# Optimization experiments

Measured on AMD Instinct MI355X. Metric: run time of the kernel, lower is better.

The kernel has to match this reference:

```python
import jax, jax.numpy as jnp
import numpy as np

L, D, H, DFF, WIN, NS = 6, 1024, 16, 4096, 5, 8
HD = D // H
EPS = 1e-5


def setup_inputs() -> dict:
    key = jax.random.key(0)
    ks = iter(jax.random.split(key, 32))
    std = 0.02
    inp = {
        "x": jax.random.normal(next(ks), (2, 1024, D), dtype=jnp.float32),
        "Wqkv": jax.random.normal(next(ks), (L, D, 3 * D), dtype=jnp.float32) * std,
        "bqkv": jnp.zeros((L, 3 * D), jnp.float32),
        "Wo": jax.random.normal(next(ks), (L, D, D), dtype=jnp.float32) * std,
        "bo": jnp.zeros((L, D), jnp.float32),
        "ln1_w": jnp.ones((L, D), jnp.float32),
        "ln1_b": jnp.zeros((L, D), jnp.float32),
        "W1": jax.random.normal(next(ks), (L, D, DFF), dtype=jnp.float32) * std,
        "b1": jnp.zeros((L, DFF), jnp.float32),
        "W2": jax.random.normal(next(ks), (L, DFF, D), dtype=jnp.float32) * std,
        "b2": jnp.zeros((L, D), jnp.float32),
        "ln2_w": jnp.ones((L, D), jnp.float32),
        "ln2_b": jnp.zeros((L, D), jnp.float32),
        "lnf_w": jnp.ones((D,), jnp.float32),
        "lnf_b": jnp.zeros((D,), jnp.float32),
        "Wp": jax.random.normal(next(ks), (D, WIN), dtype=jnp.float32) * std,
        "bp": jnp.zeros((WIN,), jnp.float32),
    }
    return inp


def _ln(x, w, b):
    mu = jnp.mean(x, axis=-1, keepdims=True)
    var = jnp.var(x, axis=-1, keepdims=True)
    return (x - mu) * jax.lax.rsqrt(var + EPS) * w + b


def reference(x, Wqkv, bqkv, Wo, bo, ln1_w, ln1_b, W1, b1, W2, b2,
              ln2_w, ln2_b, lnf_w, lnf_b, Wp, bp):
    B, S, _ = x.shape
    scale = HD ** -0.5
    causal = jnp.triu(jnp.ones((S, S), jnp.bool_), k=1)  # True = masked

    def layer(h, p):
        (wqkv, b_qkv, wo, b_o, l1w, l1b, w1, b_1, w2, b_2, l2w, l2b) = p
        # pre-norm attention
        hn = _ln(h, l1w, l1b)
        qkv = hn @ wqkv + b_qkv                       # (B,S,3D)
        qkv = qkv.reshape(B, S, 3, H, HD)
        q, k, v = (jnp.moveaxis(qkv, 2, 0)[i].transpose(0, 2, 1, 3) for i in range(3))  # (B,H,S,HD)
        scores = jnp.einsum('bhqd,bhkd->bhqk', q, k) * scale
        scores = jnp.where(causal, -jnp.inf, scores)
        probs = jax.nn.softmax(scores, axis=-1)
        o = jnp.einsum('bhqk,bhkd->bhqd', probs, v)   # (B,H,S,HD)
        o = o.transpose(0, 2, 1, 3).reshape(B, S, D)
        h = h + (o @ wo + b_o)
        # pre-norm FFN (exact GELU, matching torch F.gelu default)
        hn = _ln(h, l2w, l2b)
        ff = jax.nn.gelu(hn @ w1 + b_1, approximate=False) @ w2 + b_2
        return h + ff, None

    params = (Wqkv, bqkv, Wo, bo, ln1_w, ln1_b, W1, b1, W2, b2, ln2_w, ln2_b)
    x, _ = jax.lax.scan(layer, x, params)
    x = _ln(x, lnf_w, lnf_b)
    pred = x @ Wp + bp
    # unflatten seq -> (num_windows, num_streams)
    return pred.reshape(B, S // NS, NS, WIN)
```

## Files before the change

kernel.cpp:

```cpp
#include <hip/hip_runtime.h>

typedef __attribute__((ext_vector_type(8))) __bf16 bf16x8;
typedef __attribute__((ext_vector_type(4))) __bf16 bf16x4;
typedef __attribute__((ext_vector_type(4))) float f32x4;
typedef __attribute__((ext_vector_type(8))) unsigned short u16x8;

static __device__ __forceinline__ unsigned short f2bf(float x) {
    __bf16 h = (__bf16)x;
    return __builtin_bit_cast(unsigned short, h);
}

__global__ __launch_bounds__(256) void copy_f32(const float* __restrict__ x,
                                                float* __restrict__ h, int n) {
    int i = blockIdx.x * 256 + threadIdx.x;
    if (i < n) h[i] = x[i];
}

__global__ __launch_bounds__(256) void transpose_w(const float* __restrict__ in,
                                                   __bf16* __restrict__ out,
                                                   int K, int N) {
    __shared__ __bf16 tile[32][33];
    int n0 = blockIdx.x * 32, k0 = blockIdx.y * 32;
    int tx = threadIdx.x & 31, ty = threadIdx.x >> 5;
#pragma unroll
    for (int i = 0; i < 4; ++i) {
        int r = ty + i * 8;
        tile[r][tx] = (__bf16)in[(size_t)(k0 + r) * N + n0 + tx];
    }
    __syncthreads();
#pragma unroll
    for (int i = 0; i < 4; ++i) {
        int r = ty + i * 8;
        out[(size_t)(n0 + r) * K + k0 + tx] = tile[tx][r];
    }
}

template <typename T>
__global__ __launch_bounds__(256) void ln_kernel(const float* __restrict__ in,
                                                 const float* __restrict__ w,
                                                 const float* __restrict__ b,
                                                 T* __restrict__ out) {
    int row = blockIdx.x, tid = threadIdx.x;
    const float* x = in + (size_t)row * 1024;
    float v[4], s = 0.f, ss = 0.f;
#pragma unroll
    for (int i = 0; i < 4; i++) {
        v[i] = x[tid + i * 256];
        s += v[i];
        ss += v[i] * v[i];
    }
#pragma unroll
    for (int off = 32; off >= 1; off >>= 1) {
        s  += __shfl_xor(s, off, 64);
        ss += __shfl_xor(ss, off, 64);
    }
    __shared__ float ps[4], pss[4];
    int wid = tid >> 6, lane = tid & 63;
    if (lane == 0) { ps[wid] = s; pss[wid] = ss; }
    __syncthreads();
    s  = ps[0] + ps[1] + ps[2] + ps[3];
    ss = pss[0] + pss[1] + pss[2] + pss[3];
    float mean = s * (1.f / 1024.f);
    float var  = ss * (1.f / 1024.f) - mean * mean;
    float rstd = rsqrtf(var + 1e-5f);
    T* y = out + (size_t)row * 1024;
#pragma unroll
    for (int i = 0; i < 4; i++) {
        int c = tid + i * 256;
        y[c] = (T)((v[i] - mean) * rstd * w[c] + b[c]);
    }
}

typedef const __attribute__((address_space(1))) char gas_char;
typedef __attribute__((address_space(3))) char las_char;

template <int BM, bool GELU_ACT, bool OUT_BF16, bool ATOMIC>
__global__ __launch_bounds__(256, 4) void gemm_glds(const __bf16* __restrict__ A,
                                                    const __bf16* __restrict__ BT,
                                                    const float* __restrict__ bias,
                                                    float* __restrict__ Cf,
                                                    __bf16* __restrict__ Cb,
                                                    int M, int N, int K, int kchunk) {
    constexpr int MI = BM / 32;
    __shared__ __align__(16) __bf16 As[BM * 64];
    __shared__ __align__(16) __bf16 Bs[128 * 64];
    const int tid = threadIdx.x;
    const int wave = tid >> 6, lane = tid & 63;
    const int quad = lane >> 4, l16 = lane & 15;
    const int wr = wave >> 1, wc = wave & 1;
    const int row0 = blockIdx.y * BM, col0 = blockIdx.x * 128;
    const int kbeg = blockIdx.z * kchunk, kend = kbeg + kchunk;
    const int wbase = tid & 192;

    f32x4 acc[MI][4];
#pragma unroll
    for (int mi = 0; mi < MI; ++mi)
#pragma unroll
        for (int ni = 0; ni < 4; ++ni) acc[mi][ni] = (f32x4)0.f;

    for (int k0 = kbeg; k0 < kend; k0 += 64) {
        __syncthreads();
#pragma unroll
        for (int i = 0; i < BM / 32; ++i) {
            int id = i * 256 + tid;
            int r = id >> 3, kc = (id & 7) * 8;
            __builtin_amdgcn_global_load_lds(
                (gas_char*)&A[(size_t)(row0 + r) * K + k0 + kc],
                (las_char*)&As[(size_t)(i * 256 + wbase) * 8], 16, 0, 0);
        }
#pragma unroll
        for (int i = 0; i < 4; ++i) {
            int id = i * 256 + tid;
            int r = id >> 3, kc = (id & 7) * 8;
            __builtin_amdgcn_global_load_lds(
                (gas_char*)&BT[(size_t)(col0 + r) * K + k0 + kc],
                (las_char*)&Bs[(size_t)(i * 256 + wbase) * 8], 16, 0, 0);
        }
        __syncthreads();
#pragma unroll
        for (int kk = 0; kk < 64; kk += 32) {
            bf16x8 af[MI], bfr[4];
#pragma unroll
            for (int mi = 0; mi < MI; ++mi)
                af[mi] = *(const bf16x8*)&As[(wr * (BM / 2) + mi * 16 + l16) * 64 + kk + quad * 8];
#pragma unroll
            for (int ni = 0; ni < 4; ++ni)
                bfr[ni] = *(const bf16x8*)&Bs[(wc * 64 + ni * 16 + l16) * 64 + kk + quad * 8];
#pragma unroll
            for (int mi = 0; mi < MI; ++mi)
#pragma unroll
                for (int ni = 0; ni < 4; ++ni)
                    acc[mi][ni] = __builtin_amdgcn_mfma_f32_16x16x32_bf16(
                        af[mi], bfr[ni], acc[mi][ni], 0, 0, 0);
        }
    }

#pragma unroll
    for (int mi = 0; mi < MI; ++mi) {
#pragma unroll
        for (int reg = 0; reg < 4; ++reg) {
            int m = row0 + wr * (BM / 2) + mi * 16 + quad * 4 + reg;
#pragma unroll
            for (int ni = 0; ni < 4; ++ni) {
                int n = col0 + wc * 64 + ni * 16 + l16;
                float v = acc[mi][ni][reg];
                if (ATOMIC) {
                    if (blockIdx.z == 0) v += bias[n];
                    atomicAdd(&Cf[(size_t)m * N + n], v);
                } else {
                    v += bias[n];
                    if (GELU_ACT) v = 0.5f * v * (1.f + erff(v * 0.70710678118f));
                    if (OUT_BF16) Cb[(size_t)m * N + n] = (__bf16)v;
                    else          Cf[(size_t)m * N + n] = v;
                }
            }
        }
    }
}

__global__ __launch_bounds__(256, 4) void attn_mfma_kernel(const __bf16* __restrict__ qkv,
                                                           __bf16* __restrict__ o) {
    const int S = 1024;
    int bx = blockIdx.x, h = blockIdx.y, b = blockIdx.z;
    int qt = (b == 0) ? (15 - bx) : bx;
    int tid = threadIdx.x;
    const int wave = tid >> 6, lane = tid & 63;
    const int quad = lane >> 4, l16 = lane & 15;
    const int wbase = tid & 192;

    __shared__ __align__(16) __bf16 Qs[64 * 64];
    __shared__ __align__(16) __bf16 Ks[64 * 64];
    __shared__ __align__(16) unsigned int Vs[64 * 36];
    __shared__ __align__(16) __bf16 Ps[4][16 * 72];

    const __bf16* base = qkv + (size_t)b * S * 3072 + h * 64;
    const __bf16* qb = base;
    const __bf16* kb = base + 1024;
    const __bf16* vb = base + 2048;
    const int q0 = qt * 64;

#pragma unroll
    for (int i = 0; i < 2; ++i) {
        int id = i * 256 + tid, r = id >> 3, cseg = id & 7;
        __builtin_amdgcn_global_load_lds(
            (gas_char*)&qb[(size_t)(q0 + r) * 3072 + ((cseg ^ (r & 7)) << 3)],
            (las_char*)&Qs[(size_t)(i * 256 + wbase) * 8], 16, 0, 0);
    }

    float m_i[4], l_i[4];
    f32x4 acc[4];
#pragma unroll
    for (int r = 0; r < 4; ++r) { m_i[r] = -1e30f; l_i[r] = 0.f; acc[r] = (f32x4)0.f; }

    const int qrow = wave * 16 + quad * 4;
    __bf16* Pw = Ps[wave];

    for (int c = 0; c <= qt; ++c) {
        const int k0 = c * 64;
        __syncthreads();
#pragma unroll
        for (int i = 0; i < 2; ++i) {
            int id = i * 256 + tid, r = id >> 3, cseg = id & 7;
            __builtin_amdgcn_global_load_lds(
                (gas_char*)&kb[(size_t)(k0 + r) * 3072 + ((cseg ^ (r & 7)) << 3)],
                (las_char*)&Ks[(size_t)(i * 256 + wbase) * 8], 16, 0, 0);
        }
        {
            int pr = tid & 31, d0 = (tid >> 5) << 3;
            u16x8 v0 = *(const u16x8*)&vb[(size_t)(k0 + 2 * pr) * 3072 + d0];
            u16x8 v1 = *(const u16x8*)&vb[(size_t)(k0 + 2 * pr + 1) * 3072 + d0];
#pragma unroll
            for (int j = 0; j < 8; ++j)
                Vs[(d0 + j) * 36 + pr] = (unsigned)v0[j] | ((unsigned)v1[j] << 16);
        }
        __syncthreads();

        f32x4 s4[4];
#pragma unroll
        for (int ni = 0; ni < 4; ++ni) s4[ni] = (f32x4)0.f;
#pragma unroll
        for (int kkk = 0; kkk < 2; ++kkk) {
            int rq = wave * 16 + l16;
            bf16x8 af = *(const bf16x8*)&Qs[rq * 64 + (((kkk * 4 + quad) ^ (rq & 7)) << 3)];
#pragma unroll
            for (int ni = 0; ni < 4; ++ni) {
                int rk = ni * 16 + l16;
                bf16x8 bfr = *(const bf16x8*)&Ks[rk * 64 + (((kkk * 4 + quad) ^ (rk & 7)) << 3)];
                s4[ni] = __builtin_amdgcn_mfma_f32_16x16x32_bf16(af, bfr, s4[ni], 0, 0, 0);
            }
        }

        float p[4][4];
        const bool diag = (c == qt);
#pragma unroll
        for (int reg = 0; reg < 4; ++reg) {
            float mx = -1e30f;
#pragma unroll
            for (int ni = 0; ni < 4; ++ni) {
                float sv = s4[ni][reg] * 0.125f;
                if (diag && (k0 + ni * 16 + l16 > q0 + qrow + reg)) sv = -1e30f;
                p[ni][reg] = sv;
                mx = fmaxf(mx, sv);
            }
#pragma unroll
            for (int off = 8; off >= 1; off >>= 1) mx = fmaxf(mx, __shfl_xor(mx, off, 64));
            float mnew = fmaxf(m_i[reg], mx);
            float alpha = __expf(m_i[reg] - mnew);
            m_i[reg] = mnew;
            float rs = 0.f;
#pragma unroll
            for (int ni = 0; ni < 4; ++ni) {
                float e = __expf(p[ni][reg] - mnew);
                p[ni][reg] = e;
                rs += e;
            }
#pragma unroll
            for (int off = 8; off >= 1; off >>= 1) rs += __shfl_xor(rs, off, 64);
            l_i[reg] = l_i[reg] * alpha + rs;
#pragma unroll
            for (int ni = 0; ni < 4; ++ni) acc[ni][reg] *= alpha;
        }

#pragma unroll
        for (int reg = 0; reg < 4; ++reg)
#pragma unroll
            for (int ni = 0; ni < 4; ++ni) {
                float pv = p[ni][reg];
                float po = __shfl_xor(pv, 1, 64);
                if ((l16 & 1) == 0) {
                    unsigned u = (unsigned)f2bf(pv) | ((unsigned)f2bf(po) << 16);
                    *(unsigned*)&Pw[(quad * 4 + reg) * 72 + ni * 16 + l16] = u;
                }
            }

        const __bf16* Vb = (const __bf16*)Vs;
#pragma unroll
        for (int kkk = 0; kkk < 2; ++kkk) {
            bf16x8 af = *(const bf16x8*)&Pw[l16 * 72 + kkk * 32 + quad * 8];
#pragma unroll
            for (int ni = 0; ni < 4; ++ni) {
                bf16x8 bfr = *(const bf16x8*)&Vb[(ni * 16 + l16) * 72 + kkk * 32 + quad * 8];
                acc[ni] = __builtin_amdgcn_mfma_f32_16x16x32_bf16(af, bfr, acc[ni], 0, 0, 0);
            }
        }
    }

#pragma unroll
    for (int reg = 0; reg < 4; ++reg) {
        float inv = 1.f / l_i[reg];
        int q = q0 + qrow + reg;
#pragma unroll
        for (int ni = 0; ni < 4; ++ni)
            o[((size_t)b * S + q) * 1024 + h * 64 + ni * 16 + l16] =
                (__bf16)(acc[ni][reg] * inv);
    }
}

__global__ __launch_bounds__(64) void proj_kernel(const float* __restrict__ hn,
                                                  const float* __restrict__ Wp,
                                                  const float* __restrict__ bp,
                                                  float* __restrict__ out) {
    int t = blockIdx.x, lane = threadIdx.x;
    const float* x = hn + (size_t)t * 1024;
    float acc[5] = {0.f, 0.f, 0.f, 0.f, 0.f};
    for (int d = lane; d < 1024; d += 64) {
        float xv = x[d];
#pragma unroll
        for (int j = 0; j < 5; j++) acc[j] += xv * Wp[d * 5 + j];
    }
#pragma unroll
    for (int j = 0; j < 5; j++)
#pragma unroll
        for (int off = 32; off >= 1; off >>= 1) acc[j] += __shfl_xor(acc[j], off, 64);
    if (lane == 0) {
#pragma unroll
        for (int j = 0; j < 5; j++)
            out[(size_t)t * 5 + j] = acc[j] + bp[j];
    }
}

extern "C" void kernel_launch(void* const* d_in, const int* in_sizes, int n_in,
                              void* d_out, int out_size, void* d_ws, size_t ws_size,
                              hipStream_t stream) {
    const float* x    = (const float*)d_in[0];
    const float* Wqkv = (const float*)d_in[1];
    const float* bqkv = (const float*)d_in[2];
    const float* Wo   = (const float*)d_in[3];
    const float* bo   = (const float*)d_in[4];
    const float* ln1w = (const float*)d_in[5];
    const float* ln1b = (const float*)d_in[6];
    const float* W1   = (const float*)d_in[7];
    const float* b1   = (const float*)d_in[8];
    const float* W2   = (const float*)d_in[9];
    const float* b2   = (const float*)d_in[10];
    const float* ln2w = (const float*)d_in[11];
    const float* ln2b = (const float*)d_in[12];
    const float* lnfw = (const float*)d_in[13];
    const float* lnfb = (const float*)d_in[14];
    const float* Wp   = (const float*)d_in[15];
    const float* bp   = (const float*)d_in[16];
    float* out = (float*)d_out;

    char* p = (char*)d_ws;
    float*  h    = (float*)p;  p += (size_t)2097152 * 4;
    __bf16* hn_b = (__bf16*)p; p += (size_t)2097152 * 2;
    float*  qkv  = (float*)p;  p += (size_t)6291456 * 4;
    __bf16* o_b  = (__bf16*)p; p += (size_t)2097152 * 2;
    __bf16* ff_b = (__bf16*)p; p += (size_t)8388608 * 2;
    __bf16* wT   = (__bf16*)p;
    __bf16* wqkvT = wT;
    __bf16* woT   = wqkvT + 3145728;
    __bf16* w1T   = woT   + 1048576;
    __bf16* w2T   = w1T   + 4194304;
    __bf16* qkv_b = (__bf16*)qkv;

    copy_f32<<<8192, 256, 0, stream>>>(x, h, 2097152);

    for (int l = 0; l < 6; ++l) {
        transpose_w<<<dim3(96, 32), 256, 0, stream>>>(Wqkv + (size_t)l * 3145728, wqkvT, 1024, 3072);
        transpose_w<<<dim3(32, 32), 256, 0, stream>>>(Wo   + (size_t)l * 1048576, woT,   1024, 1024);
        transpose_w<<<dim3(128, 32), 256, 0, stream>>>(W1  + (size_t)l * 4194304, w1T,   1024, 4096);
        transpose_w<<<dim3(32, 128), 256, 0, stream>>>(W2  + (size_t)l * 4194304, w2T,   4096, 1024);

        ln_kernel<__bf16><<<2048, 256, 0, stream>>>(h, ln1w + l * 1024, ln1b + l * 1024, hn_b);
        gemm_glds<64, false, true, false><<<dim3(24, 32, 1), 256, 0, stream>>>(
            hn_b, wqkvT, bqkv + l * 3072, nullptr, qkv_b, 2048, 3072, 1024, 1024);
        attn_mfma_kernel<<<dim3(16, 16, 2), 256, 0, stream>>>(qkv_b, o_b);
        gemm_glds<64, false, false, true><<<dim3(8, 32, 2), 256, 0, stream>>>(
            o_b, woT, bo + l * 1024, h, nullptr, 2048, 1024, 1024, 512);
        ln_kernel<__bf16><<<2048, 256, 0, stream>>>(h, ln2w + l * 1024, ln2b + l * 1024, hn_b);
        gemm_glds<64, true, true, false><<<dim3(32, 32, 1), 256, 0, stream>>>(
            hn_b, w1T, b1 + l * 4096, nullptr, ff_b, 2048, 4096, 1024, 1024);
        gemm_glds<64, false, false, true><<<dim3(8, 32, 4), 256, 0, stream>>>(
            ff_b, w2T, b2 + l * 1024, h, nullptr, 2048, 1024, 4096, 1024);
    }
    float* hn_f = qkv;
    ln_kernel<float><<<2048, 256, 0, stream>>>(h, lnfw, lnfb, hn_f);
    proj_kernel<<<2048, 64, 0, stream>>>(hn_f, Wp, bp, out);
}
```

Measured before the change: 1.509 ms.

## Fuse weight transposes into one vectorized kernel and enlarge GEMM M tiles

Result: slower. 1.549 ms (+2.6%).

```diff
diff --git a/kernel.cpp b/kernel.cpp
--- a/kernel.cpp
+++ b/kernel.cpp
@@ -16,22 +16,47 @@
     if (i < n) h[i] = x[i];
 }
 
-__global__ __launch_bounds__(256) void transpose_w(const float* __restrict__ in,
-                                                   __bf16* __restrict__ out,
-                                                   int K, int N) {
-    __shared__ __bf16 tile[32][33];
-    int n0 = blockIdx.x * 32, k0 = blockIdx.y * 32;
-    int tx = threadIdx.x & 31, ty = threadIdx.x >> 5;
-#pragma unroll
-    for (int i = 0; i < 4; ++i) {
-        int r = ty + i * 8;
-        tile[r][tx] = (__bf16)in[(size_t)(k0 + r) * N + n0 + tx];
+__global__ __launch_bounds__(256) void transpose_all(const float* __restrict__ Wqkv,
+                                                     const float* __restrict__ Wo,
+                                                     const float* __restrict__ W1,
+                                                     const float* __restrict__ W2,
+                                                     __bf16* __restrict__ wqkvT,
+                                                     __bf16* __restrict__ woT,
+                                                     __bf16* __restrict__ w1T,
+                                                     __bf16* __restrict__ w2T) {
+    int bid = blockIdx.x;
+    const float* in;
+    __bf16* out;
+    int K, N, tn, tk;
+    if (bid < 768)       { in = Wqkv; out = wqkvT; K = 1024; N = 3072; tn = bid % 48; tk = bid / 48; }
+    else if (bid < 1024) { bid -= 768;  in = Wo; out = woT;  K = 1024; N = 1024; tn = bid % 16; tk = bid / 16; }
+    else if (bid < 2048) { bid -= 1024; in = W1; out = w1T;  K = 1024; N = 4096; tn = bid % 64; tk = bid / 64; }
+    else                 { bid -= 2048; in = W2; out = w2T;  K = 4096; N = 1024; tn = bid % 16; tk = bid / 16; }
+
+    __shared__ __bf16 tile[64][72];
+    int tx = threadIdx.x & 15, ty = threadIdx.x >> 4;
+    int n0 = tn * 64, k0 = tk * 64;
+#pragma unroll
+    for (int p = 0; p < 4; ++p) {
+        int k = ty + p * 16;
+        float4 v = *(const float4*)&in[(size_t)(k0 + k) * N + n0 + tx * 4];
+#pragma unroll
+        for (int j = 0; j < 4; ++j) {
+            int n = tx * 4 + j;
+            tile[n][k ^ (((n >> 2) & 7) << 3)] = (__bf16)((&v.x)[j]);
+        }
     }
     __syncthreads();
 #pragma unroll
-    for (int i = 0; i < 4; ++i) {
-        int r = ty + i * 8;
-        out[(size_t)(n0 + r) * K + k0 + tx] = tile[tx][r];
+    for (int p = 0; p < 4; ++p) {
+        int n = ty + p * 16;
+        int ks = (tx * 4) ^ (((n >> 2) & 7) << 3);
+        bf16x4 o4;
+        o4[0] = tile[n][ks + 0];
+        o4[1] = tile[n][ks + 1];
+        o4[2] = tile[n][ks + 2];
+        o4[3] = tile[n][ks + 3];
+        *(bf16x4*)&out[(size_t)(n0 + n) * K + k0 + tx * 4] = o4;
     }
 }
 
@@ -75,7 +100,7 @@
 typedef __attribute__((address_space(3))) char las_char;
 
 template <int BM, bool GELU_ACT, bool OUT_BF16, bool ATOMIC>
-__global__ __launch_bounds__(256, 4) void gemm_glds(const __bf16* __restrict__ A,
+__global__ __launch_bounds__(256, 2) void gemm_glds(const __bf16* __restrict__ A,
                                                     const __bf16* __restrict__ BT,
                                                     const float* __restrict__ bias,
                                                     float* __restrict__ Cf,
@@ -357,21 +382,21 @@
     copy_f32<<<8192, 256, 0, stream>>>(x, h, 2097152);
 
     for (int l = 0; l < 6; ++l) {
-        transpose_w<<<dim3(96, 32), 256, 0, stream>>>(Wqkv + (size_t)l * 3145728, wqkvT, 1024, 3072);
-        transpose_w<<<dim3(32, 32), 256, 0, stream>>>(Wo   + (size_t)l * 1048576, woT,   1024, 1024);
-        transpose_w<<<dim3(128, 32), 256, 0, stream>>>(W1  + (size_t)l * 4194304, w1T,   1024, 4096);
-        transpose_w<<<dim3(32, 128), 256, 0, stream>>>(W2  + (size_t)l * 4194304, w2T,   4096, 1024);
+        transpose_all<<<3072, 256, 0, stream>>>(
+            Wqkv + (size_t)l * 3145728, Wo + (size_t)l * 1048576,
+            W1 + (size_t)l * 4194304, W2 + (size_t)l * 4194304,
+            wqkvT, woT, w1T, w2T);
 
         ln_kernel<__bf16><<<2048, 256, 0, stream>>>(h, ln1w + l * 1024, ln1b + l * 1024, hn_b);
-        gemm_glds<64, false, true, false><<<dim3(24, 32, 1), 256, 0, stream>>>(
+        gemm_glds<128, false, true, false><<<dim3(24, 16, 1), 256, 0, stream>>>(
             hn_b, wqkvT, bqkv + l * 3072, nullptr, qkv_b, 2048, 3072, 1024, 1024);
         attn_mfma_kernel<<<dim3(16, 16, 2), 256, 0, stream>>>(qkv_b, o_b);
         gemm_glds<64, false, false, true><<<dim3(8, 32, 2), 256, 0, stream>>>(
             o_b, woT, bo + l * 1024, h, nullptr, 2048, 1024, 1024, 512);
         ln_kernel<__bf16><<<2048, 256, 0, stream>>>(h, ln2w + l * 1024, ln2b + l * 1024, hn_b);
-        gemm_glds<64, true, true, false><<<dim3(32, 32, 1), 256, 0, stream>>>(
+        gemm_glds<128, true, true, false><<<dim3(32, 16, 1), 256, 0, stream>>>(
             hn_b, w1T, b1 + l * 4096, nullptr, ff_b, 2048, 4096, 1024, 1024);
-        gemm_glds<64, false, false, true><<<dim3(8, 32, 4), 256, 0, stream>>>(
+        gemm_glds<128, false, false, true><<<dim3(8, 16, 4), 256, 0, stream>>>(
             ff_b, w2T, b2 + l * 1024, h, nullptr, 2048, 1024, 4096, 1024);
     }
     float* hn_f = qkv;
```
